# Optimization experiments

Hardware: AMD Instinct MI355X
Metric: run time of the kernel (lower is better)

## Reference

```python
import jax, jax.numpy as jnp
import numpy as np

DIM = 1024
HEADS = 16
HEAD_DIM = DIM // HEADS


def setup_inputs() -> dict:
    key = jax.random.key(0)
    ks = jax.random.split(key, 9)
    x = jax.random.normal(ks[0], (2, 2048, DIM), dtype=jnp.float32)
    s = 1.0 / np.sqrt(DIM)
    Wq = jax.random.normal(ks[1], (DIM, DIM), dtype=jnp.float32) * s
    bq = jax.random.normal(ks[2], (DIM,), dtype=jnp.float32) * s
    Wk = jax.random.normal(ks[3], (DIM, DIM), dtype=jnp.float32) * s
    bk = jax.random.normal(ks[4], (DIM,), dtype=jnp.float32) * s
    Wv = jax.random.normal(ks[5], (DIM, DIM), dtype=jnp.float32) * s
    bv = jax.random.normal(ks[6], (DIM,), dtype=jnp.float32) * s
    Wo = jax.random.normal(ks[7], (DIM, DIM), dtype=jnp.float32) * s
    bo = jax.random.normal(ks[8], (DIM,), dtype=jnp.float32) * s
    return {"x": x, "Wq": Wq, "bq": bq, "Wk": Wk, "bk": bk,
            "Wv": Wv, "bv": bv, "Wo": Wo, "bo": bo}


def reference(x, Wq, bq, Wk, bk, Wv, bv, Wo, bo):
    B, S, _ = x.shape
    # projections (torch Linear: x @ W.T + b; here W stored as [in, out])
    q = x @ Wq + bq
    k = x @ Wk + bk  # context = x (self-attention)
    v = x @ Wv + bv
    # [B, H, S, Dh]
    q = q.reshape(B, S, HEADS, HEAD_DIM).transpose(0, 2, 1, 3)
    k = k.reshape(B, S, HEADS, HEAD_DIM).transpose(0, 2, 1, 3)
    v = v.reshape(B, S, HEADS, HEAD_DIM).transpose(0, 2, 1, 3)
    scores = jnp.einsum('bhqd,bhkd->bhqk', q, k) / np.sqrt(HEAD_DIM).astype(np.float32)
    weights = jax.nn.softmax(scores, axis=-1)
    emb = jnp.einsum('bhqk,bhkd->bhqd', weights, v)
    emb = emb.transpose(0, 2, 1, 3).reshape(B, S, DIM)
    return emb @ Wo + bo
```

## Files before the change

### kernel.cpp

```cpp
#include <hip/hip_runtime.h>
#include <hip/hip_bf16.h>
#include <stdint.h>

typedef __attribute__((ext_vector_type(8))) short short8;
typedef __attribute__((ext_vector_type(4))) float f32x4;
typedef __attribute__((ext_vector_type(4))) unsigned int uint4v;

#define DIMW 1024
#define HEADS 16
#define HEAD_DIM 64
#define SEQ 2048
#define BATCH 2
#define MTOK 4096
#define QKVN 3072
#define QKN 2048
#define QSCALE 0.1803368801111204f

typedef const __attribute__((address_space(1))) unsigned int* gas_u32p;
typedef __attribute__((address_space(3))) unsigned int* las_u32p;

static __device__ __forceinline__ void gl_lds16(const void* g, void* l) {
    __builtin_amdgcn_global_load_lds((gas_u32p)g, (las_u32p)l, 16, 0, 0);
}

static __device__ __forceinline__ unsigned short f2bf(float f) {
    unsigned int u = __float_as_uint(f);
    u += 0x7fffu + ((u >> 16) & 1u);
    return (unsigned short)(u >> 16);
}

__global__ void cast_x_kernel(const float* __restrict__ x, unsigned short* __restrict__ out) {
    int i = (blockIdx.x * 256 + threadIdx.x) * 8;
    float4 a = *(const float4*)(x + i);
    float4 b = *(const float4*)(x + i + 4);
    unsigned short t[8] = { f2bf(a.x), f2bf(a.y), f2bf(a.z), f2bf(a.w),
                            f2bf(b.x), f2bf(b.y), f2bf(b.z), f2bf(b.w) };
    *(uint4v*)(out + i) = *(const uint4v*)t;
}

__global__ void prep_w_kernel(const float* __restrict__ Wq, const float* __restrict__ Wk,
                              const float* __restrict__ Wv, const float* __restrict__ Wo,
                              unsigned short* __restrict__ Wqkv_t, unsigned short* __restrict__ Wo_t) {
    __shared__ float tile[64][68];
    int z = blockIdx.z;
    const float* W = (z == 0) ? Wq : (z == 1) ? Wk : (z == 2) ? Wv : Wo;
    unsigned short* out = (z < 3) ? (Wqkv_t + (size_t)z * DIMW * DIMW) : Wo_t;
    int n0 = blockIdx.x * 64, k0 = blockIdx.y * 64;
    int tid = threadIdx.x;
    for (int it = 0; it < 4; ++it) {
        int c = it * 256 + tid;
        int r = c >> 4, cg = c & 15;
        float4 v = *(const float4*)(W + (size_t)(k0 + r) * DIMW + n0 + cg * 4);
        tile[r][cg * 4 + 0] = v.x; tile[r][cg * 4 + 1] = v.y;
        tile[r][cg * 4 + 2] = v.z; tile[r][cg * 4 + 3] = v.w;
    }
    __syncthreads();
    for (int it = 0; it < 2; ++it) {
        int c = it * 256 + tid;
        int n = c >> 3, kg = c & 7;
        unsigned short tmp[8];
        #pragma unroll
        for (int j = 0; j < 8; ++j) tmp[j] = f2bf(tile[kg * 8 + j][n]);
        *(uint4v*)(out + (size_t)(n0 + n) * DIMW + k0 + kg * 8) = *(const uint4v*)tmp;
    }
}

template<int MI, bool QKV3, typename TO>
__global__ __launch_bounds__(256, 3) void gemm_bt_kernel(
    const unsigned short* __restrict__ A, const unsigned short* __restrict__ Bt,
    const float* __restrict__ b0, const float* __restrict__ b1, const float* __restrict__ b2,
    TO* __restrict__ C, unsigned short* __restrict__ Vt, int M, int N, int K, int ldc)
{
    constexpr int STAGE = MI * 32 * 64 + 128 * 64;
    constexpr int TSZ = QKV3 ? 128 * 136 : 0;
    constexpr int SMEMN = STAGE > TSZ ? STAGE : TSZ;
    __shared__ __align__(16) unsigned short Smem[SMEMN];
    unsigned short* As = Smem;
    unsigned short* Bs = Smem + MI * 32 * 64;

    int tid = threadIdx.x;
    int wave = tid >> 6, lane = tid & 63;
    int lrow = lane & 15, quad = lane >> 4;
    int bm = blockIdx.y * (MI * 32), bn = blockIdx.x * 128;
    int wm = (wave >> 1) * (MI * 16), wn = (wave & 1) * 64;
    int sw = lrow & 7;
    f32x4 acc[MI][4];
    #pragma unroll
    for (int i = 0; i < MI; ++i)
        #pragma unroll
        for (int j = 0; j < 4; ++j) acc[i][j] = (f32x4){0.f, 0.f, 0.f, 0.f};
    const unsigned short* Ap = A + (size_t)bm * K;
    const unsigned short* Bp = Bt + (size_t)bn * K;
    for (int k0 = 0; k0 < K; k0 += 64) {
        __syncthreads();
        #pragma unroll
        for (int it = 0; it < MI; ++it) {
            int c = it * 256 + tid;
            int row = c >> 3, pos = c & 7;
            gl_lds16(Ap + (size_t)row * K + k0 + (pos ^ (row & 7)) * 8, &As[c * 8]);
        }
        #pragma unroll
        for (int it = 0; it < 4; ++it) {
            int c = it * 256 + tid;
            int row = c >> 3, pos = c & 7;
            gl_lds16(Bp + (size_t)row * K + k0 + (pos ^ (row & 7)) * 8, &Bs[c * 8]);
        }
        __syncthreads();
        #pragma unroll
        for (int t = 0; t < 2; ++t) {
            short8 af[MI], bfr[4];
            #pragma unroll
            for (int mi = 0; mi < MI; ++mi)
                af[mi] = *(const short8*)&As[(wm + mi * 16 + lrow) * 64 + ((t * 4 + quad) ^ sw) * 8];
            #pragma unroll
            for (int ni = 0; ni < 4; ++ni)
                bfr[ni] = *(const short8*)&Bs[(wn + ni * 16 + lrow) * 64 + ((t * 4 + quad) ^ sw) * 8];
            #pragma unroll
            for (int mi = 0; mi < MI; ++mi)
                #pragma unroll
                for (int ni = 0; ni < 4; ++ni)
                    acc[mi][ni] = __builtin_amdgcn_mfma_f32_16x16x32_bf16(af[mi], bfr[ni], acc[mi][ni], 0, 0, 0);
        }
    }

    int sel = QKV3 ? (bn >> 10) : 0;
    if (QKV3 && sel == 2) {
        __syncthreads();
        unsigned short* T = Smem;
        #pragma unroll
        for (int ni = 0; ni < 4; ++ni) {
            int v = wn + ni * 16 + lrow;
            float bias = b2[(bn & 1023) + v];
            #pragma unroll
            for (int mi = 0; mi < MI; ++mi) {
                int s0 = wm + mi * 16 + quad * 4;
                unsigned short t4[4];
                #pragma unroll
                for (int i = 0; i < 4; ++i) t4[i] = f2bf(acc[mi][ni][i] + bias);
                *(uint2*)&T[v * 136 + s0] = *(const uint2*)t4;
            }
        }
        __syncthreads();
        int bb = bm >> 11, s_base = bm & 2047;
        #pragma unroll
        for (int it = 0; it < MI * 2; ++it) {
            int c = it * 256 + tid;
            int v = c >> (MI == 4 ? 4 : 3), ch = c & (MI == 4 ? 15 : 7);
            uint4v val = *(const uint4v*)&T[v * 136 + ch * 8];
            *(uint4v*)(Vt + ((size_t)(bb * 1024 + (bn - 2048) + v)) * SEQ + s_base + ch * 8) = val;
        }
    } else {
        const float* bp = QKV3 ? ((sel == 0) ? b0 : b1) : b0;
        float scale = (QKV3 && sel == 0) ? QSCALE : 1.0f;
        #pragma unroll
        for (int ni = 0; ni < 4; ++ni) {
            int n = bn + wn + ni * 16 + lrow;
            float bias = bp[QKV3 ? (n & 1023) : n];
            #pragma unroll
            for (int mi = 0; mi < MI; ++mi) {
                int m0 = bm + wm + mi * 16 + quad * 4;
                #pragma unroll
                for (int i = 0; i < 4; ++i) {
                    float val = (acc[mi][ni][i] + bias) * scale;
                    if constexpr (sizeof(TO) == 2) C[(size_t)(m0 + i) * ldc + n] = (TO)f2bf(val);
                    else                           C[(size_t)(m0 + i) * ldc + n] = val;
                }
            }
        }
    }
}

__global__ __launch_bounds__(256, 3) void attn_kernel(
    const unsigned short* __restrict__ Qk, const unsigned short* __restrict__ Vt,
    unsigned short* __restrict__ Op, float* __restrict__ L)
{
    __shared__ __align__(16) unsigned short Ks[128 * 64];
    __shared__ __align__(16) unsigned short Vs[64 * 128];
    __shared__ __align__(16) unsigned short Ps[4][32 * 32];
    int tid = threadIdx.x;
    int wave = tid >> 6, lane = tid & 63;
    int lrow = lane & 15, quad = lane >> 4;
    int h = blockIdx.x, qblk = blockIdx.y;
    int b = blockIdx.z >> 1, split = blockIdx.z & 1;
    int q0 = qblk * 128 + wave * 32;
    const unsigned short* Qbase = Qk + (size_t)(b * SEQ) * QKN + h * 64;
    const unsigned short* Kbase = Qk + (size_t)(b * SEQ) * QKN + 1024 + h * 64;
    const unsigned short* Vtb = Vt + (size_t)(b * 1024 + h * 64) * SEQ;

    short8 qf[2][2];
    #pragma unroll
    for (int mi = 0; mi < 2; ++mi)
        #pragma unroll
        for (int kc = 0; kc < 2; ++kc)
            qf[mi][kc] = *(const short8*)(Qbase + (size_t)(q0 + mi * 16 + lrow) * QKN + kc * 32 + quad * 8);

    f32x4 o[2][4];
    float lrun[2] = {0.f, 0.f};
    #pragma unroll
    for (int mi = 0; mi < 2; ++mi)
        #pragma unroll
        for (int ont = 0; ont < 4; ++ont) o[mi][ont] = (f32x4){0.f, 0.f, 0.f, 0.f};

    int kchunk = ((lane & 7) ^ (lane >> 3)) * 8;
    int swk = lrow & 7;
    int psw = (lrow & 6) << 2;

    int kv_lo = split * 1024;
    for (int kv0 = kv_lo; kv0 < kv_lo + 1024; kv0 += 128) {
        __syncthreads();
        #pragma unroll
        for (int it = 0; it < 4; ++it) {
            int r0 = wave * 32 + it * 8;
            gl_lds16(Kbase + (size_t)(kv0 + r0 + (lane >> 3)) * QKN + kchunk,
                     &Ks[r0 * 64 + lane * 8]);
        }
        #pragma unroll
        for (int it = 0; it < 4; ++it) {
            int d0 = wave * 16 + it * 4;
            int vc = ((lane & 15) ^ ((it * 4 + (lane >> 4)) & 15)) * 8;
            gl_lds16(Vtb + (size_t)(d0 + (lane >> 4)) * SEQ + kv0 + vc,
                     &Vs[d0 * 128 + lane * 8]);
        }
        __syncthreads();

        int p01[2][8], p23[2][8];
        #pragma unroll
        for (int half = 0; half < 2; ++half) {
            f32x4 s[2][4];
            #pragma unroll
            for (int mi = 0; mi < 2; ++mi)
                #pragma unroll
                for (int nt2 = 0; nt2 < 4; ++nt2) s[mi][nt2] = (f32x4){0.f, 0.f, 0.f, 0.f};
            #pragma unroll
            for (int nt2 = 0; nt2 < 4; ++nt2) {
                int r = (half * 4 + nt2) * 16 + lrow;
                short8 kf0 = *(const short8*)&Ks[r * 64 + (quad ^ swk) * 8];
                short8 kf1 = *(const short8*)&Ks[r * 64 + ((4 + quad) ^ swk) * 8];
                #pragma unroll
                for (int mi = 0; mi < 2; ++mi) {
                    s[mi][nt2] = __builtin_amdgcn_mfma_f32_16x16x32_bf16(kf0, qf[mi][0], s[mi][nt2], 0, 0, 0);
                    s[mi][nt2] = __builtin_amdgcn_mfma_f32_16x16x32_bf16(kf1, qf[mi][1], s[mi][nt2], 0, 0, 0);
                }
            }
            #pragma unroll
            for (int mi = 0; mi < 2; ++mi)
                #pragma unroll
                for (int nt2 = 0; nt2 < 4; ++nt2) {
                    f32x4 p;
                    #pragma unroll
                    for (int c2 = 0; c2 < 4; ++c2) {
                        p[c2] = __builtin_amdgcn_exp2f(s[mi][nt2][c2]);
                        lrun[mi] += p[c2];
                    }
                    __hip_bfloat162 a01 = __float22bfloat162_rn(float2{p[0], p[1]});
                    __hip_bfloat162 a23 = __float22bfloat162_rn(float2{p[2], p[3]});
                    p01[mi][half * 4 + nt2] = *reinterpret_cast<int*>(&a01);
                    p23[mi][half * 4 + nt2] = *reinterpret_cast<int*>(&a23);
                }
        }

        #pragma unroll
        for (int kc = 0; kc < 4; ++kc) {
            #pragma unroll
            for (int mi = 0; mi < 2; ++mi)
                #pragma unroll
                for (int h2 = 0; h2 < 2; ++h2) {
                    int nt = kc * 2 + h2;
                    uint2 pk;
                    pk.x = (unsigned int)p01[mi][nt];
                    pk.y = (unsigned int)p23[mi][nt];
                    *(uint2*)&Ps[wave][(mi * 16 + lrow) * 32 + (((h2 * 4 + quad) << 2) ^ psw)] = pk;
                }
            short8 af0 = *(const short8*)&Ps[wave][lrow * 32 + (((quad * 2) << 2) ^ psw)];
            short8 af1 = *(const short8*)&Ps[wave][(16 + lrow) * 32 + (((quad * 2) << 2) ^ psw)];
            #pragma unroll
            for (int ont = 0; ont < 4; ++ont) {
                int rv = ont * 16 + lrow;
                int pos = ((kc * 4 + quad) ^ lrow) * 8;
                short8 vf = *(const short8*)&Vs[rv * 128 + pos];
                o[0][ont] = __builtin_amdgcn_mfma_f32_16x16x32_bf16(af0, vf, o[0][ont], 0, 0, 0);
                o[1][ont] = __builtin_amdgcn_mfma_f32_16x16x32_bf16(af1, vf, o[1][ont], 0, 0, 0);
            }
        }
    }

    #pragma unroll
    for (int mi = 0; mi < 2; ++mi) {
        float l = lrun[mi];
        l += __shfl_xor(l, 16);
        l += __shfl_xor(l, 32);
        #pragma unroll
        for (int ont = 0; ont < 4; ++ont)
            #pragma unroll
            for (int c2 = 0; c2 < 4; ++c2) {
                size_t row = (size_t)((split * 2 + b) * SEQ + q0 + mi * 16 + quad * 4 + c2);
                Op[row * DIMW + h * 64 + ont * 16 + lrow] = f2bf(o[mi][ont][c2]);
            }
        if (quad == 0)
            L[(((size_t)(split * 2 + b) * 16 + h) * SEQ) + q0 + mi * 16 + lrow] = l;
    }
}

__global__ void combine_kernel(const unsigned short* __restrict__ Op,
                               const float* __restrict__ L,
                               unsigned short* __restrict__ Emb)
{
    int e = (blockIdx.x * 256 + threadIdx.x) * 4;
    int row = e >> 10, c = e & 1023, h = c >> 6;
    int b = row >> 11, q = row & 2047;
    float l1 = L[((size_t)(0 + b) * 16 + h) * SEQ + q];
    float l2 = L[((size_t)(2 + b) * 16 + h) * SEQ + q];
    float inv = 1.0f / (l1 + l2);
    uint2 o1 = *(const uint2*)(Op + e);
    uint2 o2 = *(const uint2*)(Op + 4194304 + e);
    unsigned short t[4];
    unsigned int parts1[4] = { o1.x << 16, o1.x & 0xffff0000u, o1.y << 16, o1.y & 0xffff0000u };
    unsigned int parts2[4] = { o2.x << 16, o2.x & 0xffff0000u, o2.y << 16, o2.y & 0xffff0000u };
    #pragma unroll
    for (int j = 0; j < 4; ++j) {
        float f1 = __uint_as_float(parts1[j]);
        float f2 = __uint_as_float(parts2[j]);
        t[j] = f2bf((f1 + f2) * inv);
    }
    *(uint2*)(Emb + e) = *(const uint2*)t;
}

extern "C" void kernel_launch(void* const* d_in, const int* in_sizes, int n_in,
                              void* d_out, int out_size, void* d_ws, size_t ws_size,
                              hipStream_t stream)
{
    const float* x  = (const float*)d_in[0];
    const float* Wq = (const float*)d_in[1];
    const float* bq = (const float*)d_in[2];
    const float* Wk = (const float*)d_in[3];
    const float* bk = (const float*)d_in[4];
    const float* Wv = (const float*)d_in[5];
    const float* bv = (const float*)d_in[6];
    const float* Wo = (const float*)d_in[7];
    const float* bo = (const float*)d_in[8];
    float* out = (float*)d_out;
    char* ws = (char*)d_ws;

    unsigned short* Xbf   = (unsigned short*)(ws);
    unsigned short* Wqkvt = (unsigned short*)(ws + 8388608);
    unsigned short* Wot   = (unsigned short*)(ws + 14680064);
    unsigned short* Qk    = (unsigned short*)(ws + 16777216);
    unsigned short* Vt    = (unsigned short*)(ws + 33554432);
    unsigned short* Emb   = (unsigned short*)(ws + 41943040);
    unsigned short* Op    = (unsigned short*)(ws + 50331648);
    float*          L     = (float*)(ws + 67108864);

    cast_x_kernel<<<2048, 256, 0, stream>>>(x, Xbf);
    prep_w_kernel<<<dim3(16, 16, 4), 256, 0, stream>>>(Wq, Wk, Wv, Wo, Wqkvt, Wot);
    gemm_bt_kernel<4, true, unsigned short><<<dim3(24, 32), 256, 0, stream>>>(
        Xbf, Wqkvt, bq, bk, bv, Qk, Vt, MTOK, QKVN, DIMW, QKN);
    attn_kernel<<<dim3(16, 16, 4), 256, 0, stream>>>(Qk, Vt, Op, L);
    combine_kernel<<<4096, 256, 0, stream>>>(Op, L, Emb);
    gemm_bt_kernel<2, false, float><<<dim3(8, 64), 256, 0, stream>>>(
        Emb, Wot, bo, nullptr, nullptr, out, nullptr, MTOK, DIMW, DIMW, DIMW);
}
```

Before: 215.1 us.

## Double per-wave query rows in attention and fuse x cast into weight prep

The attention kernel now gives each wave 64 query rows instead of 32, so each block covers 256 queries and the grid is halved. Each K tile loaded to LDS is reused for twice as many queries. The score and PV loops are interleaved per 32-key chunk, which keeps the live probability registers small. The x-to-bf16 cast is folded into the weight-prep launch as an extra grid slice, removing one kernel launch. The trade-off is more accumulator registers per thread and fewer attention blocks (512), which may reduce occupancy with launch bounds (256,3).

```diff
diff --git a/kernel.cpp b/kernel.cpp
--- a/kernel.cpp
+++ b/kernel.cpp
@@ -29,24 +29,30 @@
     return (unsigned short)(u >> 16);
 }
 
-__global__ void cast_x_kernel(const float* __restrict__ x, unsigned short* __restrict__ out) {
-    int i = (blockIdx.x * 256 + threadIdx.x) * 8;
-    float4 a = *(const float4*)(x + i);
-    float4 b = *(const float4*)(x + i + 4);
-    unsigned short t[8] = { f2bf(a.x), f2bf(a.y), f2bf(a.z), f2bf(a.w),
-                            f2bf(b.x), f2bf(b.y), f2bf(b.z), f2bf(b.w) };
-    *(uint4v*)(out + i) = *(const uint4v*)t;
-}
-
-__global__ void prep_w_kernel(const float* __restrict__ Wq, const float* __restrict__ Wk,
+__global__ void prep_w_kernel(const float* __restrict__ x,
+                              const float* __restrict__ Wq, const float* __restrict__ Wk,
                               const float* __restrict__ Wv, const float* __restrict__ Wo,
+                              unsigned short* __restrict__ Xbf,
                               unsigned short* __restrict__ Wqkv_t, unsigned short* __restrict__ Wo_t) {
     __shared__ float tile[64][68];
     int z = blockIdx.z;
+    int tid = threadIdx.x;
+    if (z == 4) {
+        int idx = blockIdx.y * 16 + blockIdx.x;
+        #pragma unroll
+        for (int it = 0; it < 8; ++it) {
+            int i = ((idx * 8 + it) * 256 + tid) * 8;
+            float4 a = *(const float4*)(x + i);
+            float4 b = *(const float4*)(x + i + 4);
+            unsigned short t[8] = { f2bf(a.x), f2bf(a.y), f2bf(a.z), f2bf(a.w),
+                                    f2bf(b.x), f2bf(b.y), f2bf(b.z), f2bf(b.w) };
+            *(uint4v*)(Xbf + i) = *(const uint4v*)t;
+        }
+        return;
+    }
     const float* W = (z == 0) ? Wq : (z == 1) ? Wk : (z == 2) ? Wv : Wo;
     unsigned short* out = (z < 3) ? (Wqkv_t + (size_t)z * DIMW * DIMW) : Wo_t;
     int n0 = blockIdx.x * 64, k0 = blockIdx.y * 64;
-    int tid = threadIdx.x;
     for (int it = 0; it < 4; ++it) {
         int c = it * 256 + tid;
         int r = c >> 4, cg = c & 15;
@@ -176,28 +182,28 @@
 {
     __shared__ __align__(16) unsigned short Ks[128 * 64];
     __shared__ __align__(16) unsigned short Vs[64 * 128];
-    __shared__ __align__(16) unsigned short Ps[4][32 * 32];
+    __shared__ __align__(16) unsigned short Ps[4][64 * 32];
     int tid = threadIdx.x;
     int wave = tid >> 6, lane = tid & 63;
     int lrow = lane & 15, quad = lane >> 4;
     int h = blockIdx.x, qblk = blockIdx.y;
     int b = blockIdx.z >> 1, split = blockIdx.z & 1;
-    int q0 = qblk * 128 + wave * 32;
+    int q0 = qblk * 256 + wave * 64;
     const unsigned short* Qbase = Qk + (size_t)(b * SEQ) * QKN + h * 64;
     const unsigned short* Kbase = Qk + (size_t)(b * SEQ) * QKN + 1024 + h * 64;
     const unsigned short* Vtb = Vt + (size_t)(b * 1024 + h * 64) * SEQ;
 
-    short8 qf[2][2];
-    #pragma unroll
-    for (int mi = 0; mi < 2; ++mi)
+    short8 qf[4][2];
+    #pragma unroll
+    for (int mi = 0; mi < 4; ++mi)
         #pragma unroll
         for (int kc = 0; kc < 2; ++kc)
             qf[mi][kc] = *(const short8*)(Qbase + (size_t)(q0 + mi * 16 + lrow) * QKN + kc * 32 + quad * 8);
 
-    f32x4 o[2][4];
-    float lrun[2] = {0.f, 0.f};
-    #pragma unroll
-    for (int mi = 0; mi < 2; ++mi)
+    f32x4 o[4][4];
+    float lrun[4] = {0.f, 0.f, 0.f, 0.f};
+    #pragma unroll
+    for (int mi = 0; mi < 4; ++mi)
         #pragma unroll
         for (int ont = 0; ont < 4; ++ont) o[mi][ont] = (f32x4){0.f, 0.f, 0.f, 0.f};
 
@@ -223,69 +229,55 @@
         }
         __syncthreads();
 
-        int p01[2][8], p23[2][8];
-        #pragma unroll
-        for (int half = 0; half < 2; ++half) {
-            f32x4 s[2][4];
-            #pragma unroll
-            for (int mi = 0; mi < 2; ++mi)
-                #pragma unroll
-                for (int nt2 = 0; nt2 < 4; ++nt2) s[mi][nt2] = (f32x4){0.f, 0.f, 0.f, 0.f};
-            #pragma unroll
-            for (int nt2 = 0; nt2 < 4; ++nt2) {
-                int r = (half * 4 + nt2) * 16 + lrow;
+        #pragma unroll
+        for (int kc = 0; kc < 4; ++kc) {
+            uint2 pk[4][2];
+            #pragma unroll
+            for (int g = 0; g < 2; ++g) {
+                int r = (kc * 2 + g) * 16 + lrow;
                 short8 kf0 = *(const short8*)&Ks[r * 64 + (quad ^ swk) * 8];
                 short8 kf1 = *(const short8*)&Ks[r * 64 + ((4 + quad) ^ swk) * 8];
-                #pragma unroll
-                for (int mi = 0; mi < 2; ++mi) {
-                    s[mi][nt2] = __builtin_amdgcn_mfma_f32_16x16x32_bf16(kf0, qf[mi][0], s[mi][nt2], 0, 0, 0);
-                    s[mi][nt2] = __builtin_amdgcn_mfma_f32_16x16x32_bf16(kf1, qf[mi][1], s[mi][nt2], 0, 0, 0);
+                f32x4 s[4];
+                #pragma unroll
+                for (int mi = 0; mi < 4; ++mi) {
+                    s[mi] = (f32x4){0.f, 0.f, 0.f, 0.f};
+                    s[mi] = __builtin_amdgcn_mfma_f32_16x16x32_bf16(kf0, qf[mi][0], s[mi], 0, 0, 0);
+                    s[mi] = __builtin_amdgcn_mfma_f32_16x16x32_bf16(kf1, qf[mi][1], s[mi], 0, 0, 0);
                 }
-            }
-            #pragma unroll
-            for (int mi = 0; mi < 2; ++mi)
-                #pragma unroll
-                for (int nt2 = 0; nt2 < 4; ++nt2) {
-                    f32x4 p;
-                    #pragma unroll
-                    for (int c2 = 0; c2 < 4; ++c2) {
-                        p[c2] = __builtin_amdgcn_exp2f(s[mi][nt2][c2]);
-                        lrun[mi] += p[c2];
-                    }
-                    __hip_bfloat162 a01 = __float22bfloat162_rn(float2{p[0], p[1]});
-                    __hip_bfloat162 a23 = __float22bfloat162_rn(float2{p[2], p[3]});
-                    p01[mi][half * 4 + nt2] = *reinterpret_cast<int*>(&a01);
-                    p23[mi][half * 4 + nt2] = *reinterpret_cast<int*>(&a23);
+                #pragma unroll
+                for (int mi = 0; mi < 4; ++mi) {
+                    float p0 = __builtin_amdgcn_exp2f(s[mi][0]);
+                    float p1 = __builtin_amdgcn_exp2f(s[mi][1]);
+                    float p2 = __builtin_amdgcn_exp2f(s[mi][2]);
+                    float p3 = __builtin_amdgcn_exp2f(s[mi][3]);
+                    lrun[mi] += (p0 + p1) + (p2 + p3);
+                    __hip_bfloat162 a01 = __float22bfloat162_rn(float2{p0, p1});
+                    __hip_bfloat162 a23 = __float22bfloat162_rn(float2{p2, p3});
+                    pk[mi][g].x = *reinterpret_cast<unsigned int*>(&a01);
+                    pk[mi][g].y = *reinterpret_cast<unsigned int*>(&a23);
                 }
-        }
-
-        #pragma unroll
-        for (int kc = 0; kc < 4; ++kc) {
-            #pragma unroll
-            for (int mi = 0; mi < 2; ++mi)
-                #pragma unroll
-                for (int h2 = 0; h2 < 2; ++h2) {
-                    int nt = kc * 2 + h2;
-                    uint2 pk;
-                    pk.x = (unsigned int)p01[mi][nt];
-                    pk.y = (unsigned int)p23[mi][nt];
-                    *(uint2*)&Ps[wave][(mi * 16 + lrow) * 32 + (((h2 * 4 + quad) << 2) ^ psw)] = pk;
-                }
-            short8 af0 = *(const short8*)&Ps[wave][lrow * 32 + (((quad * 2) << 2) ^ psw)];
-            short8 af1 = *(const short8*)&Ps[wave][(16 + lrow) * 32 + (((quad * 2) << 2) ^ psw)];
+            }
+            #pragma unroll
+            for (int mi = 0; mi < 4; ++mi) {
+                *(uint2*)&Ps[wave][(mi * 16 + lrow) * 32 + ((quad << 2) ^ psw)] = pk[mi][0];
+                *(uint2*)&Ps[wave][(mi * 16 + lrow) * 32 + (((4 + quad) << 2) ^ psw)] = pk[mi][1];
+            }
+            short8 af[4];
+            #pragma unroll
+            for (int mi = 0; mi < 4; ++mi)
+                af[mi] = *(const short8*)&Ps[wave][(mi * 16 + lrow) * 32 + (((quad * 2) << 2) ^ psw)];
             #pragma unroll
             for (int ont = 0; ont < 4; ++ont) {
-                int rv = ont * 16 + lrow;
-                int pos = ((kc * 4 + quad) ^ lrow) * 8;
-                short8 vf = *(const short8*)&Vs[rv * 128 + pos];
-                o[0][ont] = __builtin_amdgcn_mfma_f32_16x16x32_bf16(af0, vf, o[0][ont], 0, 0, 0);
-                o[1][ont] = __builtin_amdgcn_mfma_f32_16x16x32_bf16(af1, vf, o[1][ont], 0, 0, 0);
-            }
-        }
-    }
-
-    #pragma unroll
-    for (int mi = 0; mi < 2; ++mi) {
+                short8 vf = *(const short8*)&Vs[(ont * 16 + lrow) * 128 + ((kc * 4 + quad) ^ lrow) * 8];
+                #pragma unroll
+                for (int mi = 0; mi < 4; ++mi)
+                    o[mi][ont] = __builtin_amdgcn_mfma_f32_16x16x32_bf16(af[mi], vf, o[mi][ont], 0, 0, 0);
+            }
+        }
+    }
+
+    #pragma unroll
+    for (int mi = 0; mi < 4; ++mi) {
         float l = lrun[mi];
         l += __shfl_xor(l, 16);
         l += __shfl_xor(l, 32);
@@ -350,11 +342,10 @@
     unsigned short* Op    = (unsigned short*)(ws + 50331648);
     float*          L     = (float*)(ws + 67108864);
 
-    cast_x_kernel<<<2048, 256, 0, stream>>>(x, Xbf);
-    prep_w_kernel<<<dim3(16, 16, 4), 256, 0, stream>>>(Wq, Wk, Wv, Wo, Wqkvt, Wot);
+    prep_w_kernel<<<dim3(16, 16, 5), 256, 0, stream>>>(x, Wq, Wk, Wv, Wo, Xbf, Wqkvt, Wot);
     gemm_bt_kernel<4, true, unsigned short><<<dim3(24, 32), 256, 0, stream>>>(
         Xbf, Wqkvt, bq, bk, bv, Qk, Vt, MTOK, QKVN, DIMW, QKN);
-    attn_kernel<<<dim3(16, 16, 4), 256, 0, stream>>>(Qk, Vt, Op, L);
+    attn_kernel<<<dim3(16, 8, 4), 256, 0, stream>>>(Qk, Vt, Op, L);
     combine_kernel<<<4096, 256, 0, stream>>>(Op, L, Emb);
     gemm_bt_kernel<2, false, float><<<dim3(8, 64), 256, 0, stream>>>(
         Emb, Wot, bo, nullptr, nullptr, out, nullptr, MTOK, DIMW, DIMW, DIMW);
```

Measured after the change: 260.8 us. +21.3%, slower.
